# Kernel optimization log

Measured on AMD Instinct MI355X. Metric: run time of the kernel, lower is better.

## Reference

```python
import jax, jax.numpy as jnp
import numpy as np

V = 50257      # vocab size
H = 512        # hidden size
S = 128        # source length
BEAM = 5       # beam width (matches beam_width=5 default)
TMAX = 32      # MAX_LENGTH decode cap
SOS, EOS = 1, 2
NEG = -1e9


def setup_inputs() -> dict:
    key = jax.random.key(0)
    ks = jax.random.split(key, 12)
    p = lambda k, shape: jax.random.normal(k, shape, jnp.float32) * 0.02
    return {
        "input_tokens": jax.random.randint(ks[0], (S,), 0, V),
        "embedding": p(ks[1], (V, H)),
        "enc_Wih": p(ks[2], (3 * H, H)),
        "enc_Whh": p(ks[3], (3 * H, H)),
        "enc_bih": jnp.zeros((3 * H,), jnp.float32),
        "enc_bhh": jnp.zeros((3 * H,), jnp.float32),
        "dec_Wih": p(ks[4], (3 * H, H)),
        "dec_Whh": p(ks[5], (3 * H, H)),
        "dec_bih": jnp.zeros((3 * H,), jnp.float32),
        "dec_bhh": jnp.zeros((3 * H,), jnp.float32),
        "W_concat": p(ks[6], (2 * H, H)),
        "W_vocab": p(ks[7], (H, V)),
    }


def gru_cell(x, h, Wih, Whh, bih, bhh):
    # x, h: [..., H]
    gi = x @ Wih.T + bih
    gh = h @ Whh.T + bhh
    ir, iz, inn = jnp.split(gi, 3, -1)
    hr, hz, hn = jnp.split(gh, 3, -1)
    r = jax.nn.sigmoid(ir + hr)
    z = jax.nn.sigmoid(iz + hz)
    n = jnp.tanh(inn + r * hn)
    return (1.0 - z) * n + z * h


def reference(input_tokens, embedding, enc_Wih, enc_Whh, enc_bih, enc_bhh,
              dec_Wih, dec_Whh, dec_bih, dec_bhh, W_concat, W_vocab):
    # ---- encoder: 1-layer GRU over source tokens ----
    src_emb = embedding[input_tokens]                       # [S, H]

    def enc_step(h, x):
        h2 = gru_cell(x, h, enc_Wih, enc_Whh, enc_bih, enc_bhh)
        return h2, h2

    enc_h, enc_out = jax.lax.scan(enc_step, jnp.zeros((H,), src_emb.dtype), src_emb)
    # enc_out: [S, H], enc_h: [H]

    def decode_step(tokens, hidden):
        # tokens: [B] int, hidden: [B, H]
        x = embedding[tokens]                               # [B, H]
        h = gru_cell(x, hidden, dec_Wih, dec_Whh, dec_bih, dec_bhh)
        attn = jax.nn.softmax(h @ enc_out.T, axis=-1)       # [B, S] Luong dot attention
        ctx = attn @ enc_out                                # [B, H]
        o = jnp.tanh(jnp.concatenate([h, ctx], -1) @ W_concat)
        logp = jax.nn.log_softmax(o @ W_vocab, axis=-1)     # [B, V]
        return logp, h

    # ---- batched beam search (GPU-resident equivalent of the heapq loop) ----
    tokens0 = jnp.full((BEAM,), SOS, jnp.int32)
    hidden0 = jnp.tile(enc_h[None], (BEAM, 1))
    scores0 = jnp.full((BEAM,), NEG, jnp.float32).at[0].set(0.0)
    fin0 = jnp.zeros((BEAM,), bool)
    len0 = jnp.ones((BEAM,), jnp.int32)
    seqs0 = jnp.zeros((BEAM, TMAX), jnp.int32)
    fin_row = jnp.full((V,), NEG, jnp.float32).at[EOS].set(0.0)

    def beam_step(state, t):
        tokens, hidden, scores, finished, lengths, seqs = state
        logp, h2 = decode_step(tokens, hidden)              # [BEAM, V]
        step_lp = jnp.where(finished[:, None], fin_row[None, :], logp)
        cand = scores[:, None] + step_lp                    # [BEAM, V]
        top_scores, flat = jax.lax.top_k(cand.reshape(-1), BEAM)
        parent = flat // V
        tok = (flat % V).astype(jnp.int32)
        par_fin = finished[parent]
        new_fin = par_fin | (tok == EOS)
        new_len = lengths[parent] + jnp.where(par_fin, 0, 1)
        new_seqs = seqs[parent].at[:, t].set(jnp.where(par_fin, 0, tok))
        return (tok, h2[parent], top_scores, new_fin, new_len, new_seqs), None

    state, _ = jax.lax.scan(beam_step, (tokens0, hidden0, scores0, fin0, len0, seqs0),
                            jnp.arange(TMAX))
    _, _, scores, _, lengths, seqs = state
    # length-normalized ranking, matching node.logp / node.leng sort
    norm = scores / lengths.astype(scores.dtype)
    order = jnp.argsort(-norm)
    return seqs[order], norm[order]
```

## Files before the change

kernel.cpp:

```cpp
#include <hip/hip_runtime.h>
#include <cstdint>
#include <cstddef>

#define V_SZ 50257
#define H_SZ 512
#define S_SZ 128
#define NBEAM 5
#define TMAXX 32
#define TOK_SOS 1
#define TOK_EOS 2
#define NEGINF (-1e9f)

#define GW 128
#define NT 512
#define GENC 16
#define COLS_PER_WG 393

#define BI_LEAF(l)  ((l)*32)
#define BI_ROOT     256
#define BI_REL(l)   (512 + (l)*32)
#define BI_ECNT     1024
#define BI_EREL     1056

#define OF_GI    0
#define OF_ENC   196608
#define OF_EW    262144
#define OF_H2    327680
#define OF_AL    332800
#define OF_OTOP  333440
#define OF_PV    336000
#define OF_PM    339200
#define OF_PS    339840
#define OF_SC    340480
#define OI_BASE  340488

template <typename T>
__device__ __forceinline__ T aload(const T* p){
  return __hip_atomic_load((T*)p, __ATOMIC_RELAXED, __HIP_MEMORY_SCOPE_AGENT);
}
template <typename T>
__device__ __forceinline__ void astore(T* p, T v){
  __hip_atomic_store(p, v, __ATOMIC_RELAXED, __HIP_MEMORY_SCOPE_AGENT);
}

__device__ __forceinline__ float wredsum(float a){
#pragma unroll
  for (int m = 32; m; m >>= 1) a += __shfl_xor(a, m, 64);
  return a;
}

template <typename F>
__device__ __forceinline__ void dbar(int* bi, int wid, F&& tail){
  __shared__ int s_last;
  int mygen = 0;
  __syncthreads();
  if (threadIdx.x == 0){
    int leaf = wid >> 4;
    mygen = aload(bi + BI_REL(leaf));
    __builtin_amdgcn_s_waitcnt(0);
    int lo = __hip_atomic_fetch_add(bi + BI_LEAF(leaf), 1, __ATOMIC_RELAXED, __HIP_MEMORY_SCOPE_AGENT);
    int last = 0;
    if (lo == 15){
      astore(bi + BI_LEAF(leaf), 0);
      __builtin_amdgcn_s_waitcnt(0);
      int ro = __hip_atomic_fetch_add(bi + BI_ROOT, 1, __ATOMIC_RELAXED, __HIP_MEMORY_SCOPE_AGENT);
      if (ro == (GW/16) - 1){
        astore(bi + BI_ROOT, 0);
        last = 1;
      }
    }
    if (!last){
      while (aload(bi + BI_REL(leaf)) == mygen) __builtin_amdgcn_s_sleep(4);
    }
    s_last = last;
  }
  __syncthreads();
  if (s_last){
    tail();
    __syncthreads();
    if (threadIdx.x == 0){
      __builtin_amdgcn_s_waitcnt(0);
#pragma unroll
      for (int l = 0; l < GW/16; ++l) astore(bi + BI_REL(l), mygen + 1);
    }
  }
  __syncthreads();
}

__global__ __launch_bounds__(256)
void k_gi(const int* __restrict__ toks, const float* __restrict__ emb,
          const float* __restrict__ eWih, const float* __restrict__ ebih,
          float* __restrict__ ws)
{
  float* fb = ws + 2048;
  float* gi = fb + OF_GI;
  const int tid = threadIdx.x, wid = blockIdx.x, lane = tid & 63, wvi = tid >> 6;
  int Wg = wid*4 + wvi;
  for (int it = 0; it < 192; ++it){
    int idx = Wg*192 + it;
    int s = idx / 1536, j = idx - s*1536;
    const float* er = emb + (size_t)toks[s]*H_SZ;
    const float* wr = eWih + (size_t)j*H_SZ;
    float a = 0.f;
#pragma unroll
    for (int u = 0; u < 8; ++u) a += er[u*64+lane]*wr[u*64+lane];
    a = wredsum(a);
    if (lane == 0) gi[idx] = a + ebih[j];
  }
  if (wid == 0){
    float* sc = fb + OF_SC;
    int* ib = (int*)(fb + OI_BASE);
    if (tid < NBEAM){
      sc[tid] = (tid==0) ? 0.f : NEGINF;
      ib[3200+tid] = TOK_SOS; ib[3208+tid] = 0; ib[3216+tid] = 1; ib[3224+tid] = 0;
    }
    for (int q = tid; q < 2*NBEAM*TMAXX; q += 256) ib[3232+q] = 0;
  }
}

__global__ __launch_bounds__(NT, 1)
void k_enc(const float* __restrict__ eWhh, const float* __restrict__ ebhh,
           float* __restrict__ ws)
{
  int* bi = (int*)ws;
  float* fb = ws + 2048;
  float* gi = fb + OF_GI;
  float* enc = fb + OF_ENC;
  const int tid = threadIdx.x, wid = blockIdx.x, lane = tid & 63, wvi = tid >> 6;
  const int i0 = wid*32;
  __shared__ float smF[96];

  float wreg[12][8];
#pragma unroll
  for (int dd = 0; dd < 12; ++dd){
    int d = wvi*12 + dd, g = d >> 5, il = d & 31;
    const float* wr = eWhh + (size_t)(g*512 + i0 + il)*H_SZ;
#pragma unroll
    for (int u = 0; u < 8; ++u) wreg[dd][u] = wr[u*64+lane];
  }

  for (int s = 0; s < S_SZ; ++s){
    float hreg[8];
    if (s == 0){
#pragma unroll
      for (int u = 0; u < 8; ++u) hreg[u] = 0.f;
    } else {
      const float* hp = enc + (size_t)(s-1)*H_SZ;
#pragma unroll
      for (int u = 0; u < 8; ++u) hreg[u] = aload(hp + u*64 + lane);
    }
#pragma unroll
    for (int dd = 0; dd < 12; ++dd){
      float a = 0.f;
#pragma unroll
      for (int u = 0; u < 8; ++u) a += wreg[dd][u]*hreg[u];
      a = wredsum(a);
      if (lane == 0) smF[wvi*12 + dd] = a;
    }
    __syncthreads();
    if (tid < 32){
      int i = i0 + tid;
      float gr = smF[tid], gz = smF[32+tid], gn = smF[64+tid];
      float gir = gi[s*1536 + i], giz = gi[s*1536 + 512 + i], gin = gi[s*1536 + 1024 + i];
      float hprev = (s==0) ? 0.f : aload(enc + (s-1)*H_SZ + i);
      float r = 1.f/(1.f + expf(-(gir + gr + ebhh[i])));
      float z = 1.f/(1.f + expf(-(giz + gz + ebhh[512+i])));
      float n = tanhf(gin + r*(gn + ebhh[1024+i]));
      astore(enc + s*H_SZ + i, (1.f - z)*n + z*hprev);
    }
    __syncthreads();
    if (tid == 0){
      int g = aload(bi + BI_EREL);
      __builtin_amdgcn_s_waitcnt(0);
      int lo = __hip_atomic_fetch_add(bi + BI_ECNT, 1, __ATOMIC_RELAXED, __HIP_MEMORY_SCOPE_AGENT);
      if (lo == GENC - 1){
        astore(bi + BI_ECNT, 0);
        __builtin_amdgcn_s_waitcnt(0);
        astore(bi + BI_EREL, g + 1);
      } else {
        while (aload(bi + BI_EREL) == g) __builtin_amdgcn_s_sleep(2);
      }
    }
    __syncthreads();
  }
}

__global__ __launch_bounds__(NT)
void k_ew(const float* __restrict__ Wc, float* __restrict__ ws)
{
  float* fb = ws + 2048;
  float* enc = fb + OF_ENC;
  float* EW  = fb + OF_EW;
  const int tid = threadIdx.x, wid = blockIdx.x;
  int jc = wid & 15, sb = wid >> 4;
  int jl = tid & 31, sl = (tid >> 5) & 15;
  int s = sb*16 + sl, j = jc*32 + jl;
  const float* er = enc + (size_t)s*H_SZ;
  const float* wc = Wc + (size_t)512*H_SZ;
  float a = 0.f;
  for (int k = 0; k < 512; ++k) a += er[k]*wc[(size_t)k*H_SZ + j];
  EW[s*H_SZ + j] = a;
}

__global__ __launch_bounds__(NT, 1)
void k_dec(const float* __restrict__ emb,
           const float* __restrict__ dWih, const float* __restrict__ dWhh,
           const float* __restrict__ dbih, const float* __restrict__ dbhh,
           const float* __restrict__ Wc,  const float* __restrict__ Wv,
           float* __restrict__ out, float* __restrict__ ws)
{
  const int wid = blockIdx.x, tid = threadIdx.x;
  const int lane = tid & 63, wvi = tid >> 6;
  int* bi = (int*)ws;
  float* fb = ws + 2048;
  float* enc  = fb + OF_ENC;
  float* EW   = fb + OF_EW;
  float* h2   = fb + OF_H2;
  float* al   = fb + OF_AL;
  float* otop = fb + OF_OTOP;
  float* pv   = fb + OF_PV;
  float* pm   = fb + OF_PM;
  float* ps   = fb + OF_PS;
  float* sc   = fb + OF_SC;
  int* ib   = (int*)(fb + OI_BASE);
  int* pidx = ib;
  int* tokA = ib + 3200;
  int* finA = ib + 3208;
  int* lenA = ib + 3216;
  int* parA = ib + 3224;
  int* seqA = ib + 3232;

  __shared__ float smF[1024];
  __shared__ int   smI[256];
  __shared__ float s_buf[2560];
  __shared__ float s_pp[648];

  for (int t = 0; t < TMAXX; ++t){
    float* h2new = h2 + (t & 1)*2560;
    float* h2old = h2 + ((t & 1) ^ 1)*2560;

    if (tid < NBEAM){ smI[tid] = aload(tokA + tid); smI[8 + tid] = t ? aload(parA + tid) : 0; }
    __syncthreads();
    if (t == 0){
      for (int q = tid; q < 2560; q += NT) s_buf[q] = enc[127*H_SZ + (q & 511)];
    } else {
      for (int q = tid; q < 2560; q += NT){
        int b = q >> 9;
        s_buf[q] = aload(h2old + smI[8 + b]*H_SZ + (q & 511));
      }
    }
    __syncthreads();
    {
      int i0 = wid*4;
      int mat = wvi >> 2;
      float srg[5][8];
      if (mat == 0){
#pragma unroll
        for (int b = 0; b < NBEAM; ++b){
          const float* sp = emb + (size_t)smI[b]*H_SZ;
#pragma unroll
          for (int u = 0; u < 8; ++u) srg[b][u] = sp[u*64+lane];
        }
      } else {
#pragma unroll
        for (int b = 0; b < NBEAM; ++b)
#pragma unroll
          for (int u = 0; u < 8; ++u) srg[b][u] = s_buf[b*512 + u*64 + lane];
      }
      for (int rr = 0; rr < 3; ++rr){
        int R = wvi*3 + rr;
        int rem = R - mat*12;
        int g = rem >> 2, il = rem & 3;
        const float* wr = ((mat==0) ? dWih : dWhh) + (size_t)(g*512 + i0 + il)*H_SZ;
        float wreg[8];
#pragma unroll
        for (int u = 0; u < 8; ++u) wreg[u] = wr[u*64+lane];
#pragma unroll
        for (int b = 0; b < NBEAM; ++b){
          float a = 0.f;
#pragma unroll
          for (int u = 0; u < 8; ++u) a += wreg[u]*srg[b][u];
          a = wredsum(a);
          if (lane == 0) smF[R*5 + b] = a;
        }
      }
      __syncthreads();
      if (tid < 20){
        int b = tid >> 2, il = tid & 3;
        int i = i0 + il;
        float ir  = smF[(0*12 + 0*4 + il)*5 + b] + dbih[i];
        float iz  = smF[(0*12 + 1*4 + il)*5 + b] + dbih[512+i];
        float inn = smF[(0*12 + 2*4 + il)*5 + b] + dbih[1024+i];
        float hr  = smF[(1*12 + 0*4 + il)*5 + b] + dbhh[i];
        float hz  = smF[(1*12 + 1*4 + il)*5 + b] + dbhh[512+i];
        float hn  = smF[(1*12 + 2*4 + il)*5 + b] + dbhh[1024+i];
        float r = 1.f/(1.f + expf(-(ir + hr)));
        float z = 1.f/(1.f + expf(-(iz + hz)));
        float n = tanhf(inn + r*hn);
        float hp = s_buf[b*512 + i];
        astore(h2new + b*H_SZ + i, (1.f - z)*n + z*hp);
      }
    }
    dbar(bi, wid, [&](){});

    for (int q = tid; q < 2560; q += NT) s_buf[q] = aload(h2new + q);
    __syncthreads();
    if (wvi < NBEAM){
      const float* er = enc + (size_t)wid*H_SZ;
      float a = 0.f;
#pragma unroll
      for (int u = 0; u < 8; ++u) a += er[u*64+lane]*s_buf[wvi*512 + u*64 + lane];
      a = wredsum(a);
      if (lane == 0) astore(al + wvi*S_SZ + wid, a);
    }
    if (tid < 320){
      int q = tid % 20, ksl = tid / 20;
      int f = wid*20 + q;
      int b = f >> 9, j = f & 511;
      float a = 0.f;
#pragma unroll 8
      for (int u = 0; u < 32; ++u){
        int k = ksl*32 + u;
        a += s_buf[b*512 + k]*Wc[(size_t)k*H_SZ + j];
      }
      smF[q*16 + ksl] = a;
    }
    __syncthreads();
    if (tid < 20){
      float a = 0.f;
#pragma unroll
      for (int u = 0; u < 16; ++u) a += smF[tid*16 + u];
      astore(otop + wid*20 + tid, a);
    }
    dbar(bi, wid, [&](){});

    if (wvi < NBEAM){
      float a1 = aload(al + wvi*S_SZ + lane), a2 = aload(al + wvi*S_SZ + 64 + lane);
      float m = fmaxf(a1, a2);
#pragma unroll
      for (int mm = 32; mm; mm >>= 1) m = fmaxf(m, __shfl_xor(m, mm, 64));
      float e1 = expf(a1 - m), e2 = expf(a2 - m);
      s_pp[wvi*128 + lane] = e1; s_pp[wvi*128 + 64 + lane] = e2;
      float ssv = wredsum(e1 + e2);
      if (lane == 0) s_pp[640 + wvi] = ssv;
    }
    __syncthreads();
    {
      float acc[5] = {0.f,0.f,0.f,0.f,0.f};
      for (int s2 = 0; s2 < 128; ++s2){
        float e = EW[(size_t)s2*H_SZ + tid];
#pragma unroll
        for (int b = 0; b < NBEAM; ++b) acc[b] += e*s_pp[b*128 + s2];
      }
#pragma unroll
      for (int b = 0; b < NBEAM; ++b)
        s_buf[b*512 + tid] = tanhf(aload(otop + b*512 + tid) + acc[b]/s_pp[640 + b]);
    }
    __syncthreads();
    {
      int vbase = wid*COLS_PER_WG;
      int v = vbase + tid;
      bool act = (tid < COLS_PER_WG) && (v < V_SZ);
      int vc = act ? v : vbase;
      const float* wp = Wv + vc;
      float a0=0.f,a1=0.f,a2=0.f,a3=0.f,a4=0.f;
      for (int hb = 0; hb < H_SZ; hb += 16){
        float wr[16];
#pragma unroll
        for (int u = 0; u < 16; ++u) wr[u] = wp[(size_t)(hb+u)*V_SZ];
#pragma unroll
        for (int u = 0; u < 16; ++u){
          float w = wr[u];
          a0 += w*s_buf[hb+u];
          a1 += w*s_buf[512+hb+u];
          a2 += w*s_buf[1024+hb+u];
          a3 += w*s_buf[1536+hb+u];
          a4 += w*s_buf[2048+hb+u];
        }
      }
      if (!act){ a0=a1=a2=a3=a4=-3e38f; }
      int myv = act ? v : 0x7FFFFFFF;
      float accs[5] = {a0,a1,a2,a3,a4};
#pragma unroll
      for (int b = 0; b < NBEAM; ++b){
        float x = accs[b];
        float m = x;
#pragma unroll
        for (int mm = 32; mm; mm >>= 1) m = fmaxf(m, __shfl_xor(m, mm, 64));
        float e = expf(x - m);
        float ssum = wredsum(e);
        float bv = x; int bc = myv;
        float w5[5]; int i5[5];
#pragma unroll
        for (int r = 0; r < 5; ++r){
          float cv2 = bv; int ci2 = bc;
#pragma unroll
          for (int mm = 32; mm; mm >>= 1){
            float ov = __shfl_xor(cv2, mm, 64); int oi = __shfl_xor(ci2, mm, 64);
            bool take = (ov > cv2) || (ov == cv2 && oi < ci2);
            cv2 = take ? ov : cv2; ci2 = take ? oi : ci2;
          }
          w5[r] = cv2; i5[r] = ci2;
          if (bc == ci2) bv = -3e38f;
        }
        if (lane == 0){
#pragma unroll
          for (int r = 0; r < 5; ++r){ smF[(wvi*5+b)*5+r] = w5[r]; smI[(wvi*5+b)*5+r] = i5[r]; }
          smF[300 + wvi*5 + b] = m;
          smF[360 + wvi*5 + b] = ssum;
        }
      }
      __syncthreads();
      if (tid < NBEAM){
        float M = -3.4e38f, Sv = 0.f;
#pragma unroll
        for (int w8 = 0; w8 < 8; ++w8){
          float m2 = smF[300 + w8*5 + tid], s2 = smF[360 + w8*5 + tid];
          if (m2 > M){ Sv = Sv*expf(M - m2) + s2; M = m2; }
          else       { Sv = Sv + s2*expf(m2 - M); }
        }
        astore(pm + wid*5 + tid, M); astore(ps + wid*5 + tid, Sv);
      }
      if (wvi < NBEAM){
        int b = wvi;
        float cval; int cidx;
        if (lane < 40){ cval = smF[((lane/5)*5 + b)*5 + (lane%5)]; cidx = smI[((lane/5)*5 + b)*5 + (lane%5)]; }
        else { cval = -3e38f; cidx = 0x7FFFFFFF; }
        float bv = cval; int bc = cidx;
#pragma unroll
        for (int r = 0; r < 5; ++r){
          float cv2 = bv; int ci2 = bc;
#pragma unroll
          for (int mm = 32; mm; mm >>= 1){
            float ov = __shfl_xor(cv2, mm, 64); int oi = __shfl_xor(ci2, mm, 64);
            bool take = (ov > cv2) || (ov == cv2 && oi < ci2);
            cv2 = take ? ov : cv2; ci2 = take ? oi : ci2;
          }
          if (lane == 0){ astore(pv + (wid*5+b)*5+r, cv2); astore(pidx + (wid*5+b)*5+r, ci2); }
          if (bc == ci2) bv = -3e38f;
        }
      }
    }
    dbar(bi, wid, [&](){
      int b5 = wvi;
      if (b5 < NBEAM){
        float m1 = aload(pm + lane*5 + b5), s1 = aload(ps + lane*5 + b5);
        float m2 = aload(pm + (64+lane)*5 + b5), s2 = aload(ps + (64+lane)*5 + b5);
        float M, Sv;
        if (m1 >= m2){ M = m1; Sv = s1 + s2*expf(m2 - m1); }
        else         { M = m2; Sv = s2 + s1*expf(m1 - m2); }
#pragma unroll
        for (int mm = 32; mm; mm >>= 1){
          float om = __shfl_xor(M, mm, 64), os = __shfl_xor(Sv, mm, 64);
          if (om > M){ Sv = Sv*expf(M - om) + os; M = om; }
          else       { Sv = Sv + os*expf(om - M); }
        }
        if (lane == 0){ smF[8 + b5] = M; smF[80 + b5] = logf(Sv); }
        float lv[5]; int li[5];
#pragma unroll
        for (int r = 0; r < 5; ++r){ lv[r] = aload(pv + (lane*5 + b5)*5 + r); li[r] = aload(pidx + (lane*5 + b5)*5 + r); }
        for (int r = 0; r < 5; ++r){
          float nv = aload(pv + ((64+lane)*5 + b5)*5 + r); int ni = aload(pidx + ((64+lane)*5 + b5)*5 + r);
          bool ins = (nv > lv[4]) || (nv == lv[4] && ni < li[4]);
          if (!ins) break;
          lv[4] = nv; li[4] = ni;
#pragma unroll
          for (int p = 4; p > 0; --p){
            bool sw = (lv[p] > lv[p-1]) || (lv[p] == lv[p-1] && li[p] < li[p-1]);
            if (sw){ float tv = lv[p]; lv[p] = lv[p-1]; lv[p-1] = tv;
                     int ti = li[p]; li[p] = li[p-1]; li[p-1] = ti; }
          }
        }
        float cv = lv[0]; int ci = li[0];
#pragma unroll
        for (int r = 0; r < 5; ++r){
          float xv = cv; int xi = ci;
#pragma unroll
          for (int mm = 32; mm; mm >>= 1){
            float ov = __shfl_xor(xv, mm, 64); int oi = __shfl_xor(xi, mm, 64);
            bool take = (ov > xv) || (ov == xv && oi < xi);
            xv = take ? ov : xv; xi = take ? oi : xi;
          }
          if (lane == 0){ smF[16 + b5*5 + r] = xv; smI[16 + b5*5 + r] = xi; }
          if (ci == xi){
            lv[0]=lv[1]; li[0]=li[1]; lv[1]=lv[2]; li[1]=li[2];
            lv[2]=lv[3]; li[2]=li[3]; lv[3]=lv[4]; li[3]=li[4];
            lv[4] = -3e38f; li[4] = 0x7FFFFFFF;
            cv = lv[0]; ci = li[0];
          }
        }
      }
      __syncthreads();
      if (wvi == 0){
        float cval = -3e38f; int cflat = 0x7FFFFFFF;
        int b = lane/5, k = lane - b*5;
        if (lane < 25){
          if (aload(finA + b)){
            if (k == 0){ cval = aload(sc + b) + 0.0f; cflat = b*V_SZ + TOK_EOS; }
          } else {
            cval = ((smF[16 + b*5 + k] - smF[8 + b]) - smF[80 + b]) + aload(sc + b);
            cflat = b*V_SZ + smI[16 + b*5 + k];
          }
        }
        float bv = cval; int bc = cflat;
#pragma unroll
        for (int r = 0; r < 5; ++r){
          float xv = bv; int xi = bc;
#pragma unroll
          for (int mm = 32; mm; mm >>= 1){
            float ov = __shfl_xor(xv, mm, 64); int oi = __shfl_xor(xi, mm, 64);
            bool take = (ov > xv) || (ov == xv && oi < xi);
            xv = take ? ov : xv; xi = take ? oi : xi;
          }
          if (lane == 0){ smF[48 + r] = xv; smI[48 + r] = xi; }
          if (bc == xi) bv = -3e38f;
        }
        if (lane < NBEAM){
          int r = lane;
          float nscore = smF[48 + r]; int nfl = smI[48 + r];
          int par = nfl / V_SZ; int tok = nfl - par*V_SZ;
          int ofin = aload(finA + par); int olen = aload(lenA + par);
          int nf = (ofin || tok == TOK_EOS) ? 1 : 0;
          int nl = olen + (ofin ? 0 : 1);
          astore(sc + r, nscore); astore(tokA + r, tok); astore(finA + r, nf);
          astore(lenA + r, nl); astore(parA + r, par);
          smI[56 + r] = par; smI[64 + r] = tok; smI[72 + r] = ofin; smI[80 + r] = nl;
          smF[56 + r] = nscore;
        }
      }
      __syncthreads();
      int cur = t & 1, nxt = 1 - cur;
      if (tid < 160){
        int r = tid >> 5, u = tid & 31;
        int par = smI[56 + r];
        int val = aload(seqA + cur*160 + par*32 + u);
        if (u == t) val = smI[72 + r] ? 0 : smI[64 + r];
        astore(seqA + nxt*160 + r*32 + u, val);
      }
      if (t == TMAXX - 1){
        __syncthreads();
        if (tid == 0){
          float nn[5];
#pragma unroll
          for (int r = 0; r < 5; ++r) nn[r] = smF[56 + r] / (float)smI[80 + r];
          int used = 0;
#pragma unroll
          for (int r = 0; r < 5; ++r){
            int best = -1;
            for (int q2 = 0; q2 < 5; ++q2){
              if (used & (1 << q2)) continue;
              if (best < 0 || nn[q2] > nn[best]) best = q2;
            }
            used |= (1 << best);
            smI[88 + r] = best; smF[64 + r] = nn[best];
          }
        }
        __syncthreads();
        if (tid < 160){
          int r = tid >> 5, u = tid & 31;
          int src = smI[88 + r];
          out[tid] = (float)aload(seqA + nxt*160 + src*32 + u);
        }
        if (tid >= 160 && tid < 165) out[tid] = smF[64 + (tid - 160)];
      }
    });
  }
}

extern "C" void kernel_launch(void* const* d_in, const int* in_sizes, int n_in,
                              void* d_out, int out_size, void* d_ws, size_t ws_size,
                              hipStream_t stream)
{
  (void)in_sizes; (void)n_in; (void)out_size; (void)ws_size;
  hipMemsetAsync(d_ws, 0, 8192, stream);
  float* ws = (float*)d_ws;
  k_gi<<<dim3(256), dim3(256), 0, stream>>>(
      (const int*)d_in[0], (const float*)d_in[1],
      (const float*)d_in[2], (const float*)d_in[4], ws);
  k_enc<<<dim3(GENC), dim3(NT), 0, stream>>>(
      (const float*)d_in[3], (const float*)d_in[5], ws);
  k_ew<<<dim3(128), dim3(NT), 0, stream>>>(
      (const float*)d_in[10], ws);
  k_dec<<<dim3(GW), dim3(NT), 0, stream>>>(
      (const float*)d_in[1],
      (const float*)d_in[6], (const float*)d_in[7],
      (const float*)d_in[8], (const float*)d_in[9],
      (const float*)d_in[10], (const float*)d_in[11],
      (float*)d_out, ws);
}
```

Measured before the change: 3.673 ms.

## Compute attention scores and concat projection redundantly per workgroup to drop a grid barrier

```diff
diff --git a/kernel.cpp b/kernel.cpp
--- a/kernel.cpp
+++ b/kernel.cpp
@@ -17,10 +17,10 @@
 #define COLS_PER_WG 393
 
 #define BI_LEAF(l)  ((l)*32)
-#define BI_ROOT     256
-#define BI_REL(l)   (512 + (l)*32)
-#define BI_ECNT     1024
-#define BI_EREL     1056
+#define BI_ROOT     544
+#define BI_REL(l)   (1024 + (l)*32)
+#define BI_ECNT     1792
+#define BI_EREL     1824
 
 #define OF_GI    0
 #define OF_ENC   196608
@@ -29,10 +29,15 @@
 #define OF_AL    332800
 #define OF_OTOP  333440
 #define OF_PV    336000
-#define OF_PM    339200
-#define OF_PS    339840
-#define OF_SC    340480
-#define OI_BASE  340488
+#define OF_PM    342400
+#define OF_PS    343680
+#define OF_SC    344960
+#define OI_BASE  344968
+#define I_TOK 6400
+#define I_FIN 6408
+#define I_LEN 6416
+#define I_PAR 6424
+#define I_SEQ 6432
 
 template <typename T>
 __device__ __forceinline__ T aload(const T* p){
@@ -112,9 +117,9 @@
     int* ib = (int*)(fb + OI_BASE);
     if (tid < NBEAM){
       sc[tid] = (tid==0) ? 0.f : NEGINF;
-      ib[3200+tid] = TOK_SOS; ib[3208+tid] = 0; ib[3216+tid] = 1; ib[3224+tid] = 0;
-    }
-    for (int q = tid; q < 2*NBEAM*TMAXX; q += 256) ib[3232+q] = 0;
+      ib[I_TOK+tid] = TOK_SOS; ib[I_FIN+tid] = 0; ib[I_LEN+tid] = 1; ib[I_PAR+tid] = 0;
+    }
+    for (int q = tid; q < 2*NBEAM*TMAXX; q += 256) ib[I_SEQ+q] = 0;
   }
 }
 
@@ -138,6 +143,11 @@
 #pragma unroll
     for (int u = 0; u < 8; ++u) wreg[dd][u] = wr[u*64+lane];
   }
+  float eb0 = 0.f, eb1 = 0.f, eb2 = 0.f;
+  if (tid < 32){
+    int i = i0 + tid;
+    eb0 = ebhh[i]; eb1 = ebhh[512+i]; eb2 = ebhh[1024+i];
+  }
 
   for (int s = 0; s < S_SZ; ++s){
     float hreg[8];
@@ -163,9 +173,9 @@
       float gr = smF[tid], gz = smF[32+tid], gn = smF[64+tid];
       float gir = gi[s*1536 + i], giz = gi[s*1536 + 512 + i], gin = gi[s*1536 + 1024 + i];
       float hprev = (s==0) ? 0.f : aload(enc + (s-1)*H_SZ + i);
-      float r = 1.f/(1.f + expf(-(gir + gr + ebhh[i])));
-      float z = 1.f/(1.f + expf(-(giz + gz + ebhh[512+i])));
-      float n = tanhf(gin + r*(gn + ebhh[1024+i]));
+      float r = 1.f/(1.f + expf(-(gir + gr + eb0)));
+      float z = 1.f/(1.f + expf(-(giz + gz + eb1)));
+      float n = tanhf(gin + r*(gn + eb2));
       astore(enc + s*H_SZ + i, (1.f - z)*n + z*hprev);
     }
     __syncthreads();
@@ -216,24 +226,25 @@
   float* enc  = fb + OF_ENC;
   float* EW   = fb + OF_EW;
   float* h2   = fb + OF_H2;
-  float* al   = fb + OF_AL;
-  float* otop = fb + OF_OTOP;
   float* pv   = fb + OF_PV;
   float* pm   = fb + OF_PM;
   float* ps   = fb + OF_PS;
   float* sc   = fb + OF_SC;
   int* ib   = (int*)(fb + OI_BASE);
   int* pidx = ib;
-  int* tokA = ib + 3200;
-  int* finA = ib + 3208;
-  int* lenA = ib + 3216;
-  int* parA = ib + 3224;
-  int* seqA = ib + 3232;
-
-  __shared__ float smF[1024];
+  int* tokA = ib + I_TOK;
+  int* finA = ib + I_FIN;
+  int* lenA = ib + I_LEN;
+  int* parA = ib + I_PAR;
+  int* seqA = ib + I_SEQ;
+
+  __shared__ float smF[512];
   __shared__ int   smI[256];
-  __shared__ float s_buf[2560];
+  __shared__ __align__(16) float s_buf[2560];
   __shared__ float s_pp[648];
+  __shared__ float s_al[640];
+
+  const int i0 = wid*4;
 
   for (int t = 0; t < TMAXX; ++t){
     float* h2new = h2 + (t & 1)*2560;
@@ -251,7 +262,6 @@
     }
     __syncthreads();
     {
-      int i0 = wid*4;
       int mat = wvi >> 2;
       float srg[5][8];
       if (mat == 0){
@@ -305,37 +315,21 @@
 
     for (int q = tid; q < 2560; q += NT) s_buf[q] = aload(h2new + q);
     __syncthreads();
-    if (wvi < NBEAM){
-      const float* er = enc + (size_t)wid*H_SZ;
-      float a = 0.f;
-#pragma unroll
-      for (int u = 0; u < 8; ++u) a += er[u*64+lane]*s_buf[wvi*512 + u*64 + lane];
-      a = wredsum(a);
-      if (lane == 0) astore(al + wvi*S_SZ + wid, a);
-    }
-    if (tid < 320){
-      int q = tid % 20, ksl = tid / 20;
-      int f = wid*20 + q;
-      int b = f >> 9, j = f & 511;
+    for (int p = tid; p < 640; p += NT){
+      int b = p >> 7, s = p & 127;
+      const float4* er4 = (const float4*)(enc + (size_t)s*H_SZ);
+      const float4* hb4 = (const float4*)(s_buf + b*512);
       float a = 0.f;
 #pragma unroll 8
-      for (int u = 0; u < 32; ++u){
-        int k = ksl*32 + u;
-        a += s_buf[b*512 + k]*Wc[(size_t)k*H_SZ + j];
-      }
-      smF[q*16 + ksl] = a;
-    }
-    __syncthreads();
-    if (tid < 20){
-      float a = 0.f;
-#pragma unroll
-      for (int u = 0; u < 16; ++u) a += smF[tid*16 + u];
-      astore(otop + wid*20 + tid, a);
-    }
-    dbar(bi, wid, [&](){});
-
+      for (int k = 0; k < 128; ++k){
+        float4 e = er4[k], h = hb4[k];
+        a += e.x*h.x + e.y*h.y + e.z*h.z + e.w*h.w;
+      }
+      s_al[p] = a;
+    }
+    __syncthreads();
     if (wvi < NBEAM){
-      float a1 = aload(al + wvi*S_SZ + lane), a2 = aload(al + wvi*S_SZ + 64 + lane);
+      float a1 = s_al[wvi*128 + lane], a2 = s_al[wvi*128 + 64 + lane];
       float m = fmaxf(a1, a2);
 #pragma unroll
       for (int mm = 32; mm; mm >>= 1) m = fmaxf(m, __shfl_xor(m, mm, 64));
@@ -344,6 +338,21 @@
       float ssv = wredsum(e1 + e2);
       if (lane == 0) s_pp[640 + wvi] = ssv;
     }
+    float atop[5] = {0.f,0.f,0.f,0.f,0.f};
+    {
+      const float* wcp = Wc + tid;
+      for (int hb = 0; hb < 512; hb += 16){
+        float wr[16];
+#pragma unroll
+        for (int u = 0; u < 16; ++u) wr[u] = wcp[(size_t)(hb+u)*H_SZ];
+#pragma unroll
+        for (int u = 0; u < 16; ++u){
+          float w = wr[u]; int h = hb + u;
+#pragma unroll
+          for (int b = 0; b < NBEAM; ++b) atop[b] += w*s_buf[b*512 + h];
+        }
+      }
+    }
     __syncthreads();
     {
       float acc[5] = {0.f,0.f,0.f,0.f,0.f};
@@ -354,7 +363,7 @@
       }
 #pragma unroll
       for (int b = 0; b < NBEAM; ++b)
-        s_buf[b*512 + tid] = tanhf(aload(otop + b*512 + tid) + acc[b]/s_pp[640 + b]);
+        s_buf[b*512 + tid] = tanhf(atop[b] + acc[b]/s_pp[640 + b]);
     }
     __syncthreads();
     {
@@ -441,6 +450,7 @@
         }
       }
     }
+
     dbar(bi, wid, [&](){
       int b5 = wvi;
       if (b5 < NBEAM){
@@ -457,13 +467,16 @@
         }
         if (lane == 0){ smF[8 + b5] = M; smF[80 + b5] = logf(Sv); }
         float lv[5]; int li[5];
-#pragma unroll
-        for (int r = 0; r < 5; ++r){ lv[r] = aload(pv + (lane*5 + b5)*5 + r); li[r] = aload(pidx + (lane*5 + b5)*5 + r); }
+        float nv5[5]; int ni5[5];
+#pragma unroll
         for (int r = 0; r < 5; ++r){
-          float nv = aload(pv + ((64+lane)*5 + b5)*5 + r); int ni = aload(pidx + ((64+lane)*5 + b5)*5 + r);
-          bool ins = (nv > lv[4]) || (nv == lv[4] && ni < li[4]);
+          lv[r]  = aload(pv + (lane*5 + b5)*5 + r);      li[r]  = aload(pidx + (lane*5 + b5)*5 + r);
+          nv5[r] = aload(pv + ((64+lane)*5 + b5)*5 + r); ni5[r] = aload(pidx + ((64+lane)*5 + b5)*5 + r);
+        }
+        for (int r = 0; r < 5; ++r){
+          bool ins = (nv5[r] > lv[4]) || (nv5[r] == lv[4] && ni5[r] < li[4]);
           if (!ins) break;
-          lv[4] = nv; li[4] = ni;
+          lv[4] = nv5[r]; li[4] = ni5[r];
 #pragma unroll
           for (int p = 4; p > 0; --p){
             bool sw = (lv[p] > lv[p-1]) || (lv[p] == lv[p-1] && li[p] < li[p-1]);
```

Result: slower. 4.927 ms (+34.2%).
